# Optimization experiments

Hardware: AMD Instinct MI355X
Metric: run time of the kernel (lower is better)

Reference implementation:

```python
import jax, jax.numpy as jnp
import numpy as np

DIM = 1024
N_HEADS = 16
HEAD_DIM = DIM // N_HEADS


def setup_inputs() -> dict:
    key = jax.random.key(0)
    k_x, k_qkv_w, k_qkv_b, k_p_w, k_p_b = jax.random.split(key, 5)
    s = 1.0 / np.sqrt(DIM)
    return {
        "x": jax.random.normal(k_x, (2, 2048, DIM), dtype=jnp.float32),
        # stored as [in, out] so forward is x @ W + b (equivalent to torch Linear)
        "qkv_w": jax.random.uniform(k_qkv_w, (DIM, 3 * DIM), minval=-s, maxval=s, dtype=jnp.float32),
        "qkv_b": jax.random.uniform(k_qkv_b, (3 * DIM,), minval=-s, maxval=s, dtype=jnp.float32),
        "proj_w": jax.random.uniform(k_p_w, (DIM, DIM), minval=-s, maxval=s, dtype=jnp.float32),
        "proj_b": jax.random.uniform(k_p_b, (DIM,), minval=-s, maxval=s, dtype=jnp.float32),
    }


def reference(x, qkv_w, qkv_b, proj_w, proj_b):
    b, s, _ = x.shape
    qkv = x @ qkv_w + qkv_b                       # [b, s, 3*dim]
    q, k, v = jnp.split(qkv, 3, axis=-1)
    def split_heads(t):
        return t.reshape(b, s, N_HEADS, HEAD_DIM).transpose(0, 2, 1, 3)  # [b, h, s, d]
    q, k, v = map(split_heads, (q, k, v))
    scale = 1.0 / np.sqrt(HEAD_DIM)
    scores = jnp.einsum("bhqd,bhkd->bhqk", q, k) * scale
    attn = jax.nn.softmax(scores, axis=-1)
    out = jnp.einsum("bhqk,bhkd->bhqd", attn, v)
    out = out.transpose(0, 2, 1, 3).reshape(b, s, DIM)
    return out @ proj_w + proj_b
```

## Files before the change

kernel.cpp:

```cpp
#include <hip/hip_runtime.h>
#include <hip/hip_bf16.h>

typedef __attribute__((ext_vector_type(8))) short bf16x8;
typedef __attribute__((ext_vector_type(4))) float f32x4;
typedef __attribute__((ext_vector_type(16))) float f32x16;
typedef __attribute__((ext_vector_type(4))) unsigned short u16x4;
typedef __attribute__((ext_vector_type(8))) unsigned short u16x8v;

#define S_LEN 2048
#define NHEAD 16
#define HDIM 64
#define DIM 1024

__device__ __forceinline__ unsigned short f2bf(float f) {
    union { float f; unsigned u; } x; x.f = f;
    unsigned r = x.u + 0x7FFFu + ((x.u >> 16) & 1u);
    return (unsigned short)(r >> 16);
}
__device__ __forceinline__ unsigned short f2bf_fast(float f) {
    union { float f; unsigned u; } x; x.f = f;
    return (unsigned short)((x.u + 0x8000u) >> 16);
}

__device__ __forceinline__ f32x4 mfma16(bf16x8 a, bf16x8 b, f32x4 c) {
    return __builtin_amdgcn_mfma_f32_16x16x32_bf16(a, b, c, 0, 0, 0);
}
__device__ __forceinline__ f32x16 mfma32(bf16x8 a, bf16x8 b, f32x16 c) {
    return __builtin_amdgcn_mfma_f32_32x32x16_bf16(a, b, c, 0, 0, 0);
}

__device__ __forceinline__ float fexp2(float x) {
#if __has_builtin(__builtin_amdgcn_exp2f)
    return __builtin_amdgcn_exp2f(x);
#else
    return exp2f(x);
#endif
}

__device__ __forceinline__ void gl_lds16(const void* g, void* l) {
    __builtin_amdgcn_global_load_lds(
        (const __attribute__((address_space(1))) unsigned int*)g,
        (__attribute__((address_space(3))) unsigned int*)l, 16, 0, 0);
}

__global__ __launch_bounds__(256) void xconv_kernel(const float* __restrict__ X,
                                                    unsigned short* __restrict__ Xb) {
    size_t i = ((size_t)blockIdx.x * 256 + threadIdx.x) * 8;
    float4 a = *reinterpret_cast<const float4*>(&X[i]);
    float4 b = *reinterpret_cast<const float4*>(&X[i + 4]);
    u16x8v o;
    o[0] = f2bf(a.x); o[1] = f2bf(a.y); o[2] = f2bf(a.z); o[3] = f2bf(a.w);
    o[4] = f2bf(b.x); o[5] = f2bf(b.y); o[6] = f2bf(b.z); o[7] = f2bf(b.w);
    *reinterpret_cast<u16x8v*>(&Xb[i]) = o;
}

__global__ __launch_bounds__(256) void wtrans_kernel(const float* __restrict__ W,
                                                     unsigned short* __restrict__ Wt,
                                                     int K, int N) {
    __shared__ float lds[64][65];
    int k0 = blockIdx.x * 64, n0 = blockIdx.y * 64;
    int tid = threadIdx.x;
    for (int idx = tid; idx < 1024; idx += 256) {
        int row = idx >> 4, c = (idx & 15) << 2;
        float4 v = *reinterpret_cast<const float4*>(&W[(size_t)(k0 + row) * N + n0 + c]);
        lds[row][c] = v.x; lds[row][c + 1] = v.y; lds[row][c + 2] = v.z; lds[row][c + 3] = v.w;
    }
    __syncthreads();
    for (int idx = tid; idx < 1024; idx += 256) {
        int row = idx >> 4, c = (idx & 15) << 2;
        u16x4 o;
        o[0] = f2bf(lds[c][row]);     o[1] = f2bf(lds[c + 1][row]);
        o[2] = f2bf(lds[c + 2][row]); o[3] = f2bf(lds[c + 3][row]);
        *reinterpret_cast<u16x4*>(&Wt[(size_t)(n0 + row) * K + k0 + c]) = o;
    }
}

template <int MODE>
__global__ __launch_bounds__(512) void gemm_kernel(
    const unsigned short* __restrict__ Ab, const unsigned short* __restrict__ Bt,
    const float* __restrict__ bias,
    unsigned short* __restrict__ Qb, unsigned short* __restrict__ Kb,
    unsigned short* __restrict__ Vt, float* __restrict__ outf) {
    __shared__ unsigned short Alds[128 * 64];
    __shared__ unsigned short Blds[128 * 64];
    const int tid = threadIdx.x;
    const int m0 = blockIdx.x * 128, n0 = blockIdx.y * 128;
    const int wid = tid >> 6, lane = tid & 63;
    const int wm = wid >> 2, wn = wid & 3;
    const int lr = lane & 15, lg = lane >> 4;

    const char* Abase = (const char*)(Ab + (size_t)m0 * 1024);
    const char* Bbase = (const char*)(Bt + (size_t)n0 * 1024);

    int srcOff[2], dstOff[2];
#pragma unroll
    for (int i = 0; i < 2; ++i) {
        int off = i * 8192 + tid * 16;
        int row = off >> 7, col = off & 127;
        srcOff[i] = row * 2048 + (col ^ ((row & 7) << 4));
        dstOff[i] = off;
    }
    const int swz = (lr & 7) << 4;

    f32x4 acc[4][2] = {};

    for (int kt = 0; kt < 16; ++kt) {
        __syncthreads();
#pragma unroll
        for (int i = 0; i < 2; ++i) {
            gl_lds16(Abase + srcOff[i] + kt * 128, (char*)Alds + dstOff[i]);
            gl_lds16(Bbase + srcOff[i] + kt * 128, (char*)Blds + dstOff[i]);
        }
        __syncthreads();

#pragma unroll
        for (int ks = 0; ks < 2; ++ks) {
            bf16x8 af[4], bfr[2];
#pragma unroll
            for (int i = 0; i < 4; ++i)
                af[i] = *reinterpret_cast<const bf16x8*>(
                    (const char*)Alds + (wm * 64 + i * 16 + lr) * 128 + ((ks * 64 + lg * 16) ^ swz));
#pragma unroll
            for (int j = 0; j < 2; ++j)
                bfr[j] = *reinterpret_cast<const bf16x8*>(
                    (const char*)Blds + (wn * 32 + j * 16 + lr) * 128 + ((ks * 64 + lg * 16) ^ swz));
            __builtin_amdgcn_s_setprio(1);
#pragma unroll
            for (int i = 0; i < 4; ++i)
#pragma unroll
                for (int j = 0; j < 2; ++j)
                    acc[i][j] = mfma16(af[i], bfr[j], acc[i][j]);
            __builtin_amdgcn_s_setprio(0);
        }
    }

    if constexpr (MODE == 0) {
        const int sec = n0 >> 10;
#pragma unroll
        for (int j = 0; j < 2; ++j) {
            int gn = n0 + wn * 32 + j * 16 + lr;
            float bv = bias[gn];
            int nn = gn & 1023, h = nn >> 6, d = nn & 63;
            if (sec == 2) {
#pragma unroll
                for (int i = 0; i < 4; ++i) {
                    int sb = m0 + wm * 64 + i * 16 + lg * 4;
                    size_t bhv = (size_t)((sb >> 11) * NHEAD + h);
                    u16x4 pv;
#pragma unroll
                    for (int r = 0; r < 4; ++r) pv[r] = f2bf(acc[i][j][r] + bv);
                    *reinterpret_cast<u16x4*>(&Vt[(bhv * HDIM + d) * S_LEN + (sb & 2047)]) = pv;
                }
            } else {
#pragma unroll
                for (int i = 0; i < 4; ++i) {
#pragma unroll
                    for (int r = 0; r < 4; ++r) {
                        int m = m0 + wm * 64 + i * 16 + lg * 4 + r;
                        int b_ = m >> 11, s_ = m & 2047;
                        size_t bh = (size_t)(b_ * NHEAD + h);
                        float v = acc[i][j][r] + bv;
                        if (sec == 0)
                            Qb[(bh * S_LEN + s_) * HDIM + d] = f2bf(v * 0.18033688f);
                        else
                            Kb[(bh * S_LEN + s_) * HDIM + d] = f2bf(v);
                    }
                }
            }
        }
    } else {
#pragma unroll
        for (int j = 0; j < 2; ++j) {
            int gn = n0 + wn * 32 + j * 16 + lr;
            float bv = bias[gn];
#pragma unroll
            for (int i = 0; i < 4; ++i) {
#pragma unroll
                for (int r = 0; r < 4; ++r) {
                    int m = m0 + wm * 64 + i * 16 + lg * 4 + r;
                    outf[(size_t)m * DIM + gn] = acc[i][j][r] + bv;
                }
            }
        }
    }
}

__device__ __forceinline__ void repack32(const f32x16& p, bf16x8 (&pa)[2]) {
#pragma unroll
    for (int k2 = 0; k2 < 2; ++k2) {
        const int rb = 8 * k2;
        unsigned aw[2], bw[2];
#pragma unroll
        for (int u = 0; u < 2; ++u) {
            unsigned a, b;
            asm("v_cvt_pk_bf16_f32 %0, %1, %2"
                : "=v"(a) : "v"(p[rb + 2 * u]), "v"(p[rb + 2 * u + 1]));
            asm("v_cvt_pk_bf16_f32 %0, %1, %2"
                : "=v"(b) : "v"(p[rb + 4 + 2 * u]), "v"(p[rb + 4 + 2 * u + 1]));
            asm volatile("v_permlane32_swap_b32 %0, %1" : "+v"(a), "+v"(b));
            aw[u] = a; bw[u] = b;
        }
        union { unsigned w[4]; bf16x8 v; } pu;
        pu.w[0] = aw[0]; pu.w[1] = aw[1]; pu.w[2] = bw[0]; pu.w[3] = bw[1];
        pa[k2] = pu.v;
    }
}

#define NPAIR 16
__global__ __launch_bounds__(512, 4) void attn_kernel(const unsigned short* __restrict__ Qb,
                                                      const unsigned short* __restrict__ Kb,
                                                      const unsigned short* __restrict__ Vt,
                                                      unsigned short* __restrict__ Ob) {
    __shared__ char smem[65536];
    const int L = blockIdx.x;
    const int xcd = L & 7, slot = L >> 3;
    const int bh = xcd + 8 * (slot & 3);
    const int qblk = slot >> 2;
    const int wid = threadIdx.x >> 6;
    const int lane = threadIdx.x & 63;
    const int l31 = lane & 31, hi = lane >> 5;
    const int qs = wid & 3, kh = wid >> 2;
    const int q0 = qblk * 128 + qs * 32;

    const unsigned short* qrow = &Qb[((size_t)bh * S_LEN + q0 + l31) * HDIM];
    bf16x8 qf[4];
#pragma unroll
    for (int kst = 0; kst < 4; ++kst)
        qf[kst] = *reinterpret_cast<const bf16x8*>(&qrow[kst * 16 + hi * 8]);

    bf16x8 onesf;
#pragma unroll
    for (int j = 0; j < 8; ++j) onesf[j] = (short)0x3F80;

    const char* kT = (const char*)&Kb[(size_t)bh * S_LEN * HDIM];
    const char* vT = (const char*)&Vt[(size_t)bh * HDIM * S_LEN];

    const char* sbase = (wid < 4) ? kT : vT;
    const int pairStride = (wid < 4) ? 16384 : 256;
    int srcOff[4], dstOff[4];
#pragma unroll
    for (int i = 0; i < 4; ++i) {
        int id = 4 * wid + i;
        if (id < 16) {
            int t2 = (id >> 3) & 1, khs = (id >> 2) & 1, kst = id & 3;
            srcOff[i] = t2 * 8192 + (khs * 32 + l31) * 128 + kst * 32 + hi * 16;
        } else {
            int c = id - 16;
            int t2 = (c >> 3) & 1, khs = (c >> 2) & 1, dt = (c >> 1) & 1, k2 = c & 1;
            srcOff[i] = t2 * 128 + (dt * 32 + l31) * 4096 + khs * 64 + k2 * 32 + hi * 16;
        }
        dstOff[i] = id * 1024;
    }

    f32x16 acc[2] = {};
    f32x16 sacc = {};

#pragma unroll
    for (int i = 0; i < 4; ++i)
        gl_lds16(sbase + srcOff[i], smem + dstOff[i]);
    __syncthreads();

    int cur = 0;
    for (int pt = 0; pt < NPAIR; ++pt) {
        if (pt + 1 < NPAIR) {
#pragma unroll
            for (int i = 0; i < 4; ++i)
                gl_lds16(sbase + (pt + 1) * pairStride + srcOff[i],
                         smem + (cur ^ 1) * 32768 + dstOff[i]);
        }
#pragma unroll
        for (int t2 = 0; t2 < 2; ++t2) {
            const char* kbb = smem + cur * 32768 + (t2 * 8 + kh * 4) * 1024 + lane * 16;
            const char* vbb = smem + cur * 32768 + 16384 + (t2 * 8 + kh * 4) * 1024 + lane * 16;

            f32x16 p = {};
            __builtin_amdgcn_s_setprio(1);
#pragma unroll
            for (int kst = 0; kst < 4; ++kst) {
                bf16x8 kb = *reinterpret_cast<const bf16x8*>(kbb + kst * 1024);
                p = mfma32(kb, qf[kst], p);
            }
            __builtin_amdgcn_s_setprio(0);

#pragma unroll
            for (int r = 0; r < 16; ++r) p[r] = fexp2(p[r]);
            bf16x8 pa[2];
            repack32(p, pa);

            __builtin_amdgcn_s_setprio(1);
            sacc = mfma32(pa[0], onesf, sacc);
            sacc = mfma32(pa[1], onesf, sacc);
#pragma unroll
            for (int dt = 0; dt < 2; ++dt)
#pragma unroll
                for (int k2 = 0; k2 < 2; ++k2) {
                    bf16x8 vb = *reinterpret_cast<const bf16x8*>(vbb + (dt * 2 + k2) * 1024);
                    acc[dt] = mfma32(pa[k2], vb, acc[dt]);
                }
            __builtin_amdgcn_s_setprio(0);
        }
        __syncthreads();
        cur ^= 1;
    }

    float* cacc = (float*)smem;
    float* cls  = (float*)(smem + 32768);
    if (kh == 1) {
#pragma unroll
        for (int dt = 0; dt < 2; ++dt)
#pragma unroll
            for (int r = 0; r < 16; ++r)
                cacc[qs * 2048 + dt * 1024 + r * 64 + lane] = acc[dt][r];
        if (l31 == 0) {
#pragma unroll
            for (int r = 0; r < 16; ++r) {
                int rq = (r & 3) + 8 * (r >> 2) + 4 * hi;
                cls[qs * 32 + rq] = sacc[r];
            }
        }
    }
    __syncthreads();
    if (kh == 0) {
#pragma unroll
        for (int dt = 0; dt < 2; ++dt)
#pragma unroll
            for (int r = 0; r < 16; ++r)
                acc[dt][r] += cacc[qs * 2048 + dt * 1024 + r * 64 + lane];

        const int b_ = bh >> 4, h = bh & 15;
        float inv[16];
#pragma unroll
        for (int r = 0; r < 16; ++r) {
            int rq = (r & 3) + 8 * (r >> 2) + 4 * hi;
            inv[r] = 1.f / (sacc[r] + cls[qs * 32 + rq]);
        }
#pragma unroll
        for (int dt = 0; dt < 2; ++dt)
#pragma unroll
            for (int r = 0; r < 16; ++r) {
                int rq = (r & 3) + 8 * (r >> 2) + 4 * hi;
                int q = q0 + rq;
                Ob[((size_t)(b_ * S_LEN + q)) * DIM + h * HDIM + dt * 32 + l31] =
                    f2bf_fast(acc[dt][r] * inv[r]);
            }
    }
}

extern "C" void kernel_launch(void* const* d_in, const int* in_sizes, int n_in,
                              void* d_out, int out_size, void* d_ws, size_t ws_size,
                              hipStream_t stream) {
    const float* x      = (const float*)d_in[0];
    const float* qkv_w  = (const float*)d_in[1];
    const float* qkv_b  = (const float*)d_in[2];
    const float* proj_w = (const float*)d_in[3];
    const float* proj_b = (const float*)d_in[4];
    float* out = (float*)d_out;

    unsigned short* Wqkvt = (unsigned short*)d_ws;
    unsigned short* Wpt   = Wqkvt + 3072 * 1024;
    unsigned short* Qb    = Wpt + 1024 * 1024;
    unsigned short* Kb    = Qb + 32 * 2048 * 64;
    unsigned short* Vt    = Kb + 32 * 2048 * 64;
    unsigned short* Ob    = Vt + 32 * 2048 * 64;
    unsigned short* Xb    = Ob + 4096 * 1024;

    xconv_kernel<<<2048, 256, 0, stream>>>(x, Xb);
    wtrans_kernel<<<dim3(16, 48), 256, 0, stream>>>(qkv_w, Wqkvt, 1024, 3072);
    wtrans_kernel<<<dim3(16, 16), 256, 0, stream>>>(proj_w, Wpt, 1024, 1024);

    gemm_kernel<0><<<dim3(32, 24), 512, 0, stream>>>(Xb, Wqkvt, qkv_b, Qb, Kb, Vt, nullptr);
    attn_kernel<<<512, 512, 0, stream>>>(Qb, Kb, Vt, Ob);
    gemm_kernel<1><<<dim3(32, 8), 512, 0, stream>>>(Ob, Wpt, proj_b, nullptr, nullptr, nullptr, out);
}
```

Baseline: 114.9 us.

## Merge prep kernels into one launch and halve attention K/V staging tile

The three preprocessing launches (x conversion and two weight transposes) are merged into one prep_kernel that picks its job from the block index, which removes two launch gaps. The attention kernel now stages 64-key tiles instead of 128-key pairs, shrinking LDS from 64 KB to about 33 KB per block. The smaller footprint lets more blocks share a CU, but it doubles the number of loop iterations and barriers. The smaller per-iteration prefetch also gives less time to hide memory latency.

```diff
diff --git a/kernel.cpp b/kernel.cpp
--- a/kernel.cpp
+++ b/kernel.cpp
@@ -43,23 +43,10 @@
         (__attribute__((address_space(3))) unsigned int*)l, 16, 0, 0);
 }
 
-__global__ __launch_bounds__(256) void xconv_kernel(const float* __restrict__ X,
-                                                    unsigned short* __restrict__ Xb) {
-    size_t i = ((size_t)blockIdx.x * 256 + threadIdx.x) * 8;
-    float4 a = *reinterpret_cast<const float4*>(&X[i]);
-    float4 b = *reinterpret_cast<const float4*>(&X[i + 4]);
-    u16x8v o;
-    o[0] = f2bf(a.x); o[1] = f2bf(a.y); o[2] = f2bf(a.z); o[3] = f2bf(a.w);
-    o[4] = f2bf(b.x); o[5] = f2bf(b.y); o[6] = f2bf(b.z); o[7] = f2bf(b.w);
-    *reinterpret_cast<u16x8v*>(&Xb[i]) = o;
-}
-
-__global__ __launch_bounds__(256) void wtrans_kernel(const float* __restrict__ W,
-                                                     unsigned short* __restrict__ Wt,
-                                                     int K, int N) {
-    __shared__ float lds[64][65];
-    int k0 = blockIdx.x * 64, n0 = blockIdx.y * 64;
-    int tid = threadIdx.x;
+__device__ __forceinline__ void wtrans_body(const float* __restrict__ W,
+                                            unsigned short* __restrict__ Wt,
+                                            int K, int N, int k0, int n0,
+                                            float (*lds)[65], int tid) {
     for (int idx = tid; idx < 1024; idx += 256) {
         int row = idx >> 4, c = (idx & 15) << 2;
         float4 v = *reinterpret_cast<const float4*>(&W[(size_t)(k0 + row) * N + n0 + c]);
@@ -72,6 +59,31 @@
         o[0] = f2bf(lds[c][row]);     o[1] = f2bf(lds[c + 1][row]);
         o[2] = f2bf(lds[c + 2][row]); o[3] = f2bf(lds[c + 3][row]);
         *reinterpret_cast<u16x4*>(&Wt[(size_t)(n0 + row) * K + k0 + c]) = o;
+    }
+}
+
+__global__ __launch_bounds__(256) void prep_kernel(const float* __restrict__ X,
+                                                   unsigned short* __restrict__ Xb,
+                                                   const float* __restrict__ Wq,
+                                                   unsigned short* __restrict__ Wqt,
+                                                   const float* __restrict__ Wp,
+                                                   unsigned short* __restrict__ Wpt) {
+    __shared__ float lds[64][65];
+    const int b = blockIdx.x, tid = threadIdx.x;
+    if (b < 2048) {
+        size_t i = ((size_t)b * 256 + tid) * 8;
+        float4 a = *reinterpret_cast<const float4*>(&X[i]);
+        float4 c = *reinterpret_cast<const float4*>(&X[i + 4]);
+        u16x8v o;
+        o[0] = f2bf(a.x); o[1] = f2bf(a.y); o[2] = f2bf(a.z); o[3] = f2bf(a.w);
+        o[4] = f2bf(c.x); o[5] = f2bf(c.y); o[6] = f2bf(c.z); o[7] = f2bf(c.w);
+        *reinterpret_cast<u16x8v*>(&Xb[i]) = o;
+    } else if (b < 2816) {
+        int idx = b - 2048;
+        wtrans_body(Wq, Wqt, 1024, 3072, (idx & 15) * 64, (idx >> 4) * 64, lds, tid);
+    } else {
+        int idx = b - 2816;
+        wtrans_body(Wp, Wpt, 1024, 1024, (idx & 15) * 64, (idx >> 4) * 64, lds, tid);
     }
 }
 
@@ -206,12 +218,12 @@
     }
 }
 
-#define NPAIR 16
+#define NT64 32
 __global__ __launch_bounds__(512, 4) void attn_kernel(const unsigned short* __restrict__ Qb,
                                                       const unsigned short* __restrict__ Kb,
                                                       const unsigned short* __restrict__ Vt,
                                                       unsigned short* __restrict__ Ob) {
-    __shared__ char smem[65536];
+    __shared__ char smem[33280];
     const int L = blockIdx.x;
     const int xcd = L & 7, slot = L >> 3;
     const int bh = xcd + 8 * (slot & 3);
@@ -236,18 +248,18 @@
     const char* vT = (const char*)&Vt[(size_t)bh * HDIM * S_LEN];
 
     const char* sbase = (wid < 4) ? kT : vT;
-    const int pairStride = (wid < 4) ? 16384 : 256;
-    int srcOff[4], dstOff[4];
-#pragma unroll
-    for (int i = 0; i < 4; ++i) {
-        int id = 4 * wid + i;
-        if (id < 16) {
-            int t2 = (id >> 3) & 1, khs = (id >> 2) & 1, kst = id & 3;
-            srcOff[i] = t2 * 8192 + (khs * 32 + l31) * 128 + kst * 32 + hi * 16;
+    const int tileStride = (wid < 4) ? 8192 : 128;
+    int srcOff[2], dstOff[2];
+#pragma unroll
+    for (int i = 0; i < 2; ++i) {
+        int id = 2 * wid + i;
+        if (id < 8) {
+            int khs = (id >> 2) & 1, kst = id & 3;
+            srcOff[i] = (khs * 32 + l31) * 128 + kst * 32 + hi * 16;
         } else {
-            int c = id - 16;
-            int t2 = (c >> 3) & 1, khs = (c >> 2) & 1, dt = (c >> 1) & 1, k2 = c & 1;
-            srcOff[i] = t2 * 128 + (dt * 32 + l31) * 4096 + khs * 64 + k2 * 32 + hi * 16;
+            int c = id - 8;
+            int khs = (c >> 2) & 1, dt = (c >> 1) & 1, k2 = c & 1;
+            srcOff[i] = (dt * 32 + l31) * 4096 + khs * 64 + k2 * 32 + hi * 16;
         }
         dstOff[i] = id * 1024;
     }
@@ -256,49 +268,48 @@
     f32x16 sacc = {};
 
 #pragma unroll
-    for (int i = 0; i < 4; ++i)
+    for (int i = 0; i < 2; ++i)
         gl_lds16(sbase + srcOff[i], smem + dstOff[i]);
     __syncthreads();
 
+    const int cofs = kh * 4096;
     int cur = 0;
-    for (int pt = 0; pt < NPAIR; ++pt) {
-        if (pt + 1 < NPAIR) {
-#pragma unroll
-            for (int i = 0; i < 4; ++i)
-                gl_lds16(sbase + (pt + 1) * pairStride + srcOff[i],
-                         smem + (cur ^ 1) * 32768 + dstOff[i]);
-        }
-#pragma unroll
-        for (int t2 = 0; t2 < 2; ++t2) {
-            const char* kbb = smem + cur * 32768 + (t2 * 8 + kh * 4) * 1024 + lane * 16;
-            const char* vbb = smem + cur * 32768 + 16384 + (t2 * 8 + kh * 4) * 1024 + lane * 16;
-
-            f32x16 p = {};
-            __builtin_amdgcn_s_setprio(1);
-#pragma unroll
-            for (int kst = 0; kst < 4; ++kst) {
-                bf16x8 kb = *reinterpret_cast<const bf16x8*>(kbb + kst * 1024);
-                p = mfma32(kb, qf[kst], p);
-            }
-            __builtin_amdgcn_s_setprio(0);
-
-#pragma unroll
-            for (int r = 0; r < 16; ++r) p[r] = fexp2(p[r]);
-            bf16x8 pa[2];
-            repack32(p, pa);
-
-            __builtin_amdgcn_s_setprio(1);
-            sacc = mfma32(pa[0], onesf, sacc);
-            sacc = mfma32(pa[1], onesf, sacc);
-#pragma unroll
-            for (int dt = 0; dt < 2; ++dt)
-#pragma unroll
-                for (int k2 = 0; k2 < 2; ++k2) {
-                    bf16x8 vb = *reinterpret_cast<const bf16x8*>(vbb + (dt * 2 + k2) * 1024);
-                    acc[dt] = mfma32(pa[k2], vb, acc[dt]);
-                }
-            __builtin_amdgcn_s_setprio(0);
-        }
+    for (int t = 0; t < NT64; ++t) {
+        if (t + 1 < NT64) {
+#pragma unroll
+            for (int i = 0; i < 2; ++i)
+                gl_lds16(sbase + (t + 1) * tileStride + srcOff[i],
+                         smem + (cur ^ 1) * 16384 + dstOff[i]);
+        }
+        const char* kbb = smem + cur * 16384 + cofs + lane * 16;
+        const char* vbb = smem + cur * 16384 + 8192 + cofs + lane * 16;
+
+        f32x16 p = {};
+        __builtin_amdgcn_s_setprio(1);
+#pragma unroll
+        for (int kst = 0; kst < 4; ++kst) {
+            bf16x8 kb = *reinterpret_cast<const bf16x8*>(kbb + kst * 1024);
+            p = mfma32(kb, qf[kst], p);
+        }
+        __builtin_amdgcn_s_setprio(0);
+
+#pragma unroll
+        for (int r = 0; r < 16; ++r) p[r] = fexp2(p[r]);
+        bf16x8 pa[2];
+        repack32(p, pa);
+
+        __builtin_amdgcn_s_setprio(1);
+        sacc = mfma32(pa[0], onesf, sacc);
+        sacc = mfma32(pa[1], onesf, sacc);
+#pragma unroll
+        for (int dt = 0; dt < 2; ++dt)
+#pragma unroll
+            for (int k2 = 0; k2 < 2; ++k2) {
+                bf16x8 vb = *reinterpret_cast<const bf16x8*>(vbb + (dt * 2 + k2) * 1024);
+                acc[dt] = mfma32(pa[k2], vb, acc[dt]);
+            }
+        __builtin_amdgcn_s_setprio(0);
+
         __syncthreads();
         cur ^= 1;
     }
@@ -364,9 +375,7 @@
     unsigned short* Ob    = Vt + 32 * 2048 * 64;
     unsigned short* Xb    = Ob + 4096 * 1024;
 
-    xconv_kernel<<<2048, 256, 0, stream>>>(x, Xb);
-    wtrans_kernel<<<dim3(16, 48), 256, 0, stream>>>(qkv_w, Wqkvt, 1024, 3072);
-    wtrans_kernel<<<dim3(16, 16), 256, 0, stream>>>(proj_w, Wpt, 1024, 1024);
+    prep_kernel<<<3072, 256, 0, stream>>>(x, Xb, qkv_w, Wqkvt, proj_w, Wpt);
 
     gemm_kernel<0><<<dim3(32, 24), 512, 0, stream>>>(Xb, Wqkvt, qkv_b, Qb, Kb, Vt, nullptr);
     attn_kernel<<<512, 512, 0, stream>>>(Qb, Kb, Vt, Ob);
```

Result: faster. 108.1 us (-5.9%).
